# Kernel tuning notes

Hardware: AMD Instinct MI355X
Metric: run time of the kernel (lower is better)

## Reference

```python
import jax, jax.numpy as jnp
import numpy as np

N_BATCH, N_SEQ, N_CHANNELS = 32, 4096, 128
N_EXPERTS, TOP_K = 64, 2
D_IN = 2 * N_SEQ  # linear input width


def setup_inputs() -> dict:
    key = jax.random.key(0)
    k_x, k_wm, k_bm, k_wn, k_bn = jax.random.split(key, 5)
    scale = 1.0 / np.sqrt(D_IN)  # torch nn.Linear default init range
    return {
        "x": jax.random.normal(k_x, (N_BATCH, N_SEQ, N_CHANNELS, 2), dtype=jnp.float32),
        "W_main": jax.random.uniform(k_wm, (N_EXPERTS, D_IN), jnp.float32, -scale, scale),
        "b_main": jax.random.uniform(k_bm, (N_EXPERTS,), jnp.float32, -scale, scale),
        "W_noise": jax.random.uniform(k_wn, (N_EXPERTS, D_IN), jnp.float32, -scale, scale),
        "b_noise": jax.random.uniform(k_bn, (N_EXPERTS,), jnp.float32, -scale, scale),
    }


def _keep_top_k(logits, k):
    # torch.kthvalue(x, n-k) = (n-k)-th smallest (1-based) = sorted[:, n-k-1]
    n = logits.shape[1]
    if n < k:
        return logits
    kth = jnp.sort(logits, axis=1)[:, n - k - 1:n - k]  # [rows, 1]
    return jnp.where(logits > kth, logits, -jnp.inf)


def reference(x, W_main, b_main, W_noise, b_noise):
    n_batch, n_seq, n_channels, _ = x.shape
    # swapaxes(1,2) then reshape -> rows=[batch*channels], feat=[seq*2]
    x_r = jnp.swapaxes(x, 1, 2).reshape(n_batch * n_channels, 2 * n_seq)
    main_out = x_r @ W_main.T + b_main                      # [rows, E]
    noise_out = jax.nn.softplus(x_r @ W_noise.T + b_noise)  # [rows, E]
    gate = _keep_top_k(main_out + noise_out, TOP_K)
    return jax.nn.softmax(gate, axis=1)
```

## Files before the change

kernel.cpp:

```cpp
#include <hip/hip_runtime.h>
#include <cmath>

typedef _Float16 f16x8 __attribute__((ext_vector_type(8)));
typedef _Float16 f16x4 __attribute__((ext_vector_type(4)));
typedef float    f32x16 __attribute__((ext_vector_type(16)));

constexpr int NBATCH = 32;
constexpr int NSEQ   = 4096;
constexpr int NCH    = 128;
constexpr int NEXP   = 64;
constexpr int NE2    = 128;
constexpr int DIN    = 2 * NSEQ;
constexpr int ROWS   = NBATCH * NCH;
constexpr int KCH    = 16;
constexpr float LOSC = 2048.0f;
constexpr float INV_LOSC = 1.0f / 2048.0f;

#define SWZ(row, k) ((((row) * 64) + (k)) ^ (((row) & 7) << 3))

__global__ __launch_bounds__(256, 2)
void gemm_kernel(const float* __restrict__ x,
                 const float* __restrict__ Wm,
                 const float* __restrict__ Wn,
                 float* __restrict__ partials)
{
    const int kc   = blockIdx.x;
    const int b    = blockIdx.y;
    const int tid  = threadIdx.x;
    const int lane = tid & 63;
    const int wave = tid >> 6;
    const int wm   = wave >> 1;
    const int wn   = wave & 1;

    __shared__ _Float16 lds[4 * 8192];
    _Float16* Ah = lds;
    _Float16* Al = lds + 8192;
    _Float16* Bh = lds + 16384;
    _Float16* Bl = lds + 24576;

    f32x16 acc1[2][2], acc2[2][2];
#pragma unroll
    for (int mi = 0; mi < 2; ++mi)
#pragma unroll
        for (int ni = 0; ni < 2; ++ni)
#pragma unroll
            for (int r = 0; r < 16; ++r) { acc1[mi][ni][r] = 0.f; acc2[mi][ni][r] = 0.f; }

    const float* xchunk = x + (size_t)b * (NSEQ * 256) + (size_t)kc * 256 * 256;
    const int fb = kc * 512;

    float2 xr[16];
    auto load_x = [&](int ss) {
        const float* bp = xchunk + ss * 8192;
#pragma unroll
        for (int u = 0; u < 4; ++u) {
            const int kg = u * 2 + (tid >> 7);
#pragma unroll
            for (int j = 0; j < 4; ++j)
                xr[u * 4 + j] = *(const float2*)(bp + (kg * 4 + j) * 256 + (tid & 127) * 2);
        }
    };

    load_x(0);

    for (int ss = 0; ss < 8; ++ss) {
        float4 wr[8];
#pragma unroll
        for (int p = 0; p < 8; ++p) {
            const int e = p * 16 + (tid >> 4);
            const float* wsrc = (e < NEXP) ? (Wm + (size_t)e * DIN)
                                           : (Wn + (size_t)(e - NEXP) * DIN);
            wr[p] = *(const float4*)(wsrc + fb + ss * 64 + (tid & 15) * 4);
        }

        if (ss) __syncthreads();

#pragma unroll
        for (int u = 0; u < 4; ++u) {
            const int kg = u * 2 + (tid >> 7);
            const int c  = tid & 127;
            f16x8 hv, lv;
#pragma unroll
            for (int i = 0; i < 8; ++i) {
                float v = (i & 1) ? xr[u * 4 + (i >> 1)].y : xr[u * 4 + (i >> 1)].x;
                _Float16 h = (_Float16)v;
                hv[i] = h;
                lv[i] = (_Float16)((v - (float)h) * LOSC);
            }
            const int hw = SWZ(c, kg * 8);
            *(f16x8*)&Ah[hw] = hv;
            *(f16x8*)&Al[hw] = lv;
        }
#pragma unroll
        for (int p = 0; p < 8; ++p) {
            const int e = p * 16 + (tid >> 4);
            float vv[4] = { wr[p].x, wr[p].y, wr[p].z, wr[p].w };
            f16x4 hv, lv;
#pragma unroll
            for (int i = 0; i < 4; ++i) {
                _Float16 h = (_Float16)vv[i];
                hv[i] = h;
                lv[i] = (_Float16)((vv[i] - (float)h) * LOSC);
            }
            const int hw = SWZ(e, (tid & 15) * 4);
            *(f16x4*)&Bh[hw] = hv;
            *(f16x4*)&Bl[hw] = lv;
        }
        __syncthreads();

        if (ss < 7) load_x(ss + 1);

#pragma unroll
        for (int kk = 0; kk < 4; ++kk) {
            const int ko = kk * 16 + (lane >> 5) * 8;
            f16x8 ah[2], al[2], bh[2], bl[2];
#pragma unroll
            for (int i = 0; i < 2; ++i) {
                const int ra = wm * 64 + i * 32 + (lane & 31);
                const int rb = wn * 64 + i * 32 + (lane & 31);
                ah[i] = *(const f16x8*)&Ah[SWZ(ra, ko)];
                al[i] = *(const f16x8*)&Al[SWZ(ra, ko)];
                bh[i] = *(const f16x8*)&Bh[SWZ(rb, ko)];
                bl[i] = *(const f16x8*)&Bl[SWZ(rb, ko)];
            }
#pragma unroll
            for (int mi = 0; mi < 2; ++mi)
#pragma unroll
                for (int ni = 0; ni < 2; ++ni) {
                    acc1[mi][ni] = __builtin_amdgcn_mfma_f32_32x32x16_f16(ah[mi], bh[ni], acc1[mi][ni], 0, 0, 0);
                    acc2[mi][ni] = __builtin_amdgcn_mfma_f32_32x32x16_f16(ah[mi], bl[ni], acc2[mi][ni], 0, 0, 0);
                    acc2[mi][ni] = __builtin_amdgcn_mfma_f32_32x32x16_f16(al[mi], bh[ni], acc2[mi][ni], 0, 0, 0);
                }
        }
    }

    float* outp = partials + ((size_t)kc * ROWS + (size_t)b * NCH) * NE2;
#pragma unroll
    for (int mi = 0; mi < 2; ++mi)
#pragma unroll
        for (int ni = 0; ni < 2; ++ni)
#pragma unroll
            for (int r = 0; r < 16; ++r) {
                const int rloc = (r & 3) + 8 * (r >> 2) + 4 * (lane >> 5);
                const int crow = wm * 64 + mi * 32 + rloc;
                const int e    = wn * 64 + ni * 32 + (lane & 31);
                outp[(size_t)crow * NE2 + e] = acc1[mi][ni][r] + acc2[mi][ni][r] * INV_LOSC;
            }
}

__global__ __launch_bounds__(256)
void gate_kernel(const float* __restrict__ partials,
                 const float* __restrict__ bm,
                 const float* __restrict__ bn,
                 float* __restrict__ out)
{
    const int tid  = threadIdx.x;
    const int rl   = tid >> 7;
    const int e    = tid & 127;
    const int lane = tid & 63;
    const int row  = blockIdx.x * 2 + rl;

    const float* p = partials + (size_t)row * NE2 + e;
    float s = 0.f;
#pragma unroll
    for (int kc = 0; kc < KCH; ++kc)
        s += p[(size_t)kc * ROWS * NE2];

    __shared__ float spl[2][64];
    if (e >= NEXP) {
        float nz = s + bn[lane];
        spl[rl][lane] = fmaxf(nz, 0.f) + log1pf(expf(-fabsf(nz)));
    }
    __syncthreads();
    if (e < NEXP) {
        float g = s + bm[lane] + spl[rl][lane];

        float v  = g;
        float m1 = v;
#pragma unroll
        for (int o = 32; o > 0; o >>= 1) m1 = fmaxf(m1, __shfl_xor(m1, o));
        unsigned long long b1 = __ballot(v == m1);
        int l1 = __ffsll(b1) - 1;
        if (lane == l1) v = -INFINITY;
        float m2 = v;
#pragma unroll
        for (int o = 32; o > 0; o >>= 1) m2 = fmaxf(m2, __shfl_xor(m2, o));
        unsigned long long b2 = __ballot(v == m2);
        int l2 = __ffsll(b2) - 1;
        if (lane == l2) v = -INFINITY;
        float kth = v;
#pragma unroll
        for (int o = 32; o > 0; o >>= 1) kth = fmaxf(kth, __shfl_xor(kth, o));

        float ev  = (g > kth) ? expf(g - m1) : 0.f;
        float den = ev;
#pragma unroll
        for (int o = 32; o > 0; o >>= 1) den += __shfl_xor(den, o);
        out[(size_t)row * NEXP + lane] = ev / den;
    }
}

extern "C" void kernel_launch(void* const* d_in, const int* in_sizes, int n_in,
                              void* d_out, int out_size, void* d_ws, size_t ws_size,
                              hipStream_t stream)
{
    const float* x  = (const float*)d_in[0];
    const float* Wm = (const float*)d_in[1];
    const float* bm = (const float*)d_in[2];
    const float* Wn = (const float*)d_in[3];
    const float* bn = (const float*)d_in[4];
    float* out      = (float*)d_out;
    float* partials = (float*)d_ws;

    dim3 g1(KCH, NBATCH);
    gemm_kernel<<<g1, 256, 0, stream>>>(x, Wm, Wn, partials);
    gate_kernel<<<ROWS / 2, 256, 0, stream>>>(partials, bm, bn, out);
}
```

Baseline: 211.9 us.

## Pre-split weights to fp16 hi/lo and double-buffer LDS with direct global-to-LDS loads

Adds a prep kernel that converts both weight matrices once into swizzled fp16 hi/lo arrays in workspace. The GEMM then streams those arrays straight into LDS with global_load_lds and uses two LDS buffers with smaller K tiles, so the next tile's loads overlap the current tile's MFMAs. Block indices are remapped so that neighbouring blocks share batch and chunk data. This removes the per-block weight conversion and the serialised load/compute steps, at the cost of an extra kernel launch and extra workspace traffic.

```diff
diff --git a/kernel.cpp b/kernel.cpp
--- a/kernel.cpp
+++ b/kernel.cpp
@@ -13,30 +13,65 @@
 constexpr int DIN    = 2 * NSEQ;
 constexpr int ROWS   = NBATCH * NCH;
 constexpr int KCH    = 16;
+constexpr int KT     = 16;
 constexpr float LOSC = 2048.0f;
 constexpr float INV_LOSC = 1.0f / 2048.0f;
 
-#define SWZ(row, k) ((((row) * 64) + (k)) ^ (((row) & 7) << 3))
+constexpr size_t WS_WHI = 32ull << 20;
+constexpr size_t WS_WLO = 34ull << 20;
+
+__device__ __forceinline__ int swz_f16(int row, int g) {
+    return row * 32 + ((g ^ ((row >> 1) & 3)) << 3);
+}
+
+__device__ __forceinline__ void gload_lds16(const void* g, void* l) {
+    __builtin_amdgcn_global_load_lds(
+        (const __attribute__((address_space(1))) unsigned int*)g,
+        (__attribute__((address_space(3))) unsigned int*)l, 16, 0, 0);
+}
+
+__global__ __launch_bounds__(256)
+void wprep_kernel(const float* __restrict__ Wm, const float* __restrict__ Wn,
+                  _Float16* __restrict__ Whi, _Float16* __restrict__ Wlo)
+{
+    const int idx = (blockIdx.x * 256 + threadIdx.x) * 4;
+    const int row = idx >> 13;
+    const int f   = idx & 8191;
+    const float* src = (row < NEXP) ? (Wm + (size_t)row * DIN + f)
+                                    : (Wn + (size_t)(row - NEXP) * DIN + f);
+    const float4 v = *(const float4*)src;
+    const int g  = (f >> 3) & 3;
+    const int fs = (f & ~0x18) | ((g ^ ((row >> 1) & 3)) << 3);
+    float vv[4] = { v.x, v.y, v.z, v.w };
+    f16x4 h, l;
+#pragma unroll
+    for (int j = 0; j < 4; ++j) {
+        _Float16 hj = (_Float16)vv[j];
+        h[j] = hj;
+        l[j] = (_Float16)((vv[j] - (float)hj) * LOSC);
+    }
+    *(f16x4*)&Whi[(size_t)row * 8192 + fs] = h;
+    *(f16x4*)&Wlo[(size_t)row * 8192 + fs] = l;
+}
 
 __global__ __launch_bounds__(256, 2)
 void gemm_kernel(const float* __restrict__ x,
-                 const float* __restrict__ Wm,
-                 const float* __restrict__ Wn,
+                 const _Float16* __restrict__ Whi,
+                 const _Float16* __restrict__ Wlo,
                  float* __restrict__ partials)
 {
-    const int kc   = blockIdx.x;
-    const int b    = blockIdx.y;
+    const int l    = blockIdx.x;
+    const int slot = l >> 3;
+    const int kc   = (l & 7) + 8 * (slot & 1);
+    const int b    = slot >> 1;
+
     const int tid  = threadIdx.x;
     const int lane = tid & 63;
     const int wave = tid >> 6;
     const int wm   = wave >> 1;
     const int wn   = wave & 1;
 
-    __shared__ _Float16 lds[4 * 8192];
-    _Float16* Ah = lds;
-    _Float16* Al = lds + 8192;
-    _Float16* Bh = lds + 16384;
-    _Float16* Bl = lds + 24576;
+    __shared__ _Float16 lds[2 * 16384];
 
     f32x16 acc1[2][2], acc2[2][2];
 #pragma unroll
@@ -46,82 +81,81 @@
 #pragma unroll
             for (int r = 0; r < 16; ++r) { acc1[mi][ni][r] = 0.f; acc2[mi][ni][r] = 0.f; }
 
-    const float* xchunk = x + (size_t)b * (NSEQ * 256) + (size_t)kc * 256 * 256;
-    const int fb = kc * 512;
-
-    float2 xr[16];
-    auto load_x = [&](int ss) {
-        const float* bp = xchunk + ss * 8192;
-#pragma unroll
-        for (int u = 0; u < 4; ++u) {
-            const int kg = u * 2 + (tid >> 7);
-#pragma unroll
-            for (int j = 0; j < 4; ++j)
-                xr[u * 4 + j] = *(const float2*)(bp + (kg * 4 + j) * 256 + (tid & 127) * 2);
+    const float* xchunk = x + (size_t)b * (NSEQ * 256) + (size_t)kc * (256 * 256);
+    const int c    = tid & 127;
+    const int gsel = tid >> 7;
+    const int fb0  = kc * 512;
+
+    const int e_ld = lane >> 2;
+    const int goff = (lane & 3) * 8;
+
+    float2 xr[8];
+    auto load_x = [&](int t) {
+#pragma unroll
+        for (int u = 0; u < 2; ++u) {
+            const int g = u * 2 + gsel;
+#pragma unroll
+            for (int i = 0; i < 4; ++i)
+                xr[u * 4 + i] = *(const float2*)(xchunk + (size_t)(t * 16 + g * 4 + i) * 256 + c * 2);
         }
     };
-
+    auto write_x = [&](int buf) {
+        _Float16* Ah = lds + buf * 16384;
+        _Float16* Al = Ah + 4096;
+#pragma unroll
+        for (int u = 0; u < 2; ++u) {
+            const int g = u * 2 + gsel;
+            f16x8 h, lo;
+#pragma unroll
+            for (int i = 0; i < 4; ++i) {
+                float a0 = xr[u * 4 + i].x, a1 = xr[u * 4 + i].y;
+                _Float16 h0 = (_Float16)a0, h1 = (_Float16)a1;
+                h[2 * i] = h0; h[2 * i + 1] = h1;
+                lo[2 * i]     = (_Float16)((a0 - (float)h0) * LOSC);
+                lo[2 * i + 1] = (_Float16)((a1 - (float)h1) * LOSC);
+            }
+            const int off = swz_f16(c, g);
+            *(f16x8*)&Ah[off] = h;
+            *(f16x8*)&Al[off] = lo;
+        }
+    };
+    auto issue_W = [&](int t, int buf) {
+        const int fb = fb0 + t * 32;
+        _Float16* Bh = lds + buf * 16384 + 8192;
+        _Float16* Bl = Bh + 4096;
+#pragma unroll
+        for (int q = 0; q < 2; ++q) {
+            const int e0 = wave * 32 + q * 16;
+            gload_lds16(Whi + (size_t)(e0 + e_ld) * 8192 + fb + goff, Bh + e0 * 32);
+            gload_lds16(Wlo + (size_t)(e0 + e_ld) * 8192 + fb + goff, Bl + e0 * 32);
+        }
+    };
+
+    issue_W(0, 0);
     load_x(0);
-
-    for (int ss = 0; ss < 8; ++ss) {
-        float4 wr[8];
-#pragma unroll
-        for (int p = 0; p < 8; ++p) {
-            const int e = p * 16 + (tid >> 4);
-            const float* wsrc = (e < NEXP) ? (Wm + (size_t)e * DIN)
-                                           : (Wn + (size_t)(e - NEXP) * DIN);
-            wr[p] = *(const float4*)(wsrc + fb + ss * 64 + (tid & 15) * 4);
-        }
-
-        if (ss) __syncthreads();
-
-#pragma unroll
-        for (int u = 0; u < 4; ++u) {
-            const int kg = u * 2 + (tid >> 7);
-            const int c  = tid & 127;
-            f16x8 hv, lv;
-#pragma unroll
-            for (int i = 0; i < 8; ++i) {
-                float v = (i & 1) ? xr[u * 4 + (i >> 1)].y : xr[u * 4 + (i >> 1)].x;
-                _Float16 h = (_Float16)v;
-                hv[i] = h;
-                lv[i] = (_Float16)((v - (float)h) * LOSC);
-            }
-            const int hw = SWZ(c, kg * 8);
-            *(f16x8*)&Ah[hw] = hv;
-            *(f16x8*)&Al[hw] = lv;
-        }
-#pragma unroll
-        for (int p = 0; p < 8; ++p) {
-            const int e = p * 16 + (tid >> 4);
-            float vv[4] = { wr[p].x, wr[p].y, wr[p].z, wr[p].w };
-            f16x4 hv, lv;
-#pragma unroll
-            for (int i = 0; i < 4; ++i) {
-                _Float16 h = (_Float16)vv[i];
-                hv[i] = h;
-                lv[i] = (_Float16)((vv[i] - (float)h) * LOSC);
-            }
-            const int hw = SWZ(e, (tid & 15) * 4);
-            *(f16x4*)&Bh[hw] = hv;
-            *(f16x4*)&Bl[hw] = lv;
-        }
-        __syncthreads();
-
-        if (ss < 7) load_x(ss + 1);
-
-#pragma unroll
-        for (int kk = 0; kk < 4; ++kk) {
-            const int ko = kk * 16 + (lane >> 5) * 8;
+    write_x(0);
+    __syncthreads();
+
+    for (int t = 0; t < KT; ++t) {
+        const int buf = t & 1;
+        if (t < KT - 1) { issue_W(t + 1, buf ^ 1); load_x(t + 1); }
+
+        const _Float16* Ah = lds + buf * 16384;
+        const _Float16* Al = Ah + 4096;
+        const _Float16* Bh = Ah + 8192;
+        const _Float16* Bl = Ah + 12288;
+#pragma unroll
+        for (int kk = 0; kk < 2; ++kk) {
+            const int gk = kk * 2 + (lane >> 5);
             f16x8 ah[2], al[2], bh[2], bl[2];
 #pragma unroll
             for (int i = 0; i < 2; ++i) {
-                const int ra = wm * 64 + i * 32 + (lane & 31);
-                const int rb = wn * 64 + i * 32 + (lane & 31);
-                ah[i] = *(const f16x8*)&Ah[SWZ(ra, ko)];
-                al[i] = *(const f16x8*)&Al[SWZ(ra, ko)];
-                bh[i] = *(const f16x8*)&Bh[SWZ(rb, ko)];
-                bl[i] = *(const f16x8*)&Bl[SWZ(rb, ko)];
+                const int oa = swz_f16(wm * 64 + i * 32 + (lane & 31), gk);
+                const int ob = swz_f16(wn * 64 + i * 32 + (lane & 31), gk);
+                ah[i] = *(const f16x8*)&Ah[oa];
+                al[i] = *(const f16x8*)&Al[oa];
+                bh[i] = *(const f16x8*)&Bh[ob];
+                bl[i] = *(const f16x8*)&Bl[ob];
             }
 #pragma unroll
             for (int mi = 0; mi < 2; ++mi)
@@ -132,6 +166,8 @@
                     acc2[mi][ni] = __builtin_amdgcn_mfma_f32_32x32x16_f16(al[mi], bh[ni], acc2[mi][ni], 0, 0, 0);
                 }
         }
+        if (t < KT - 1) write_x(buf ^ 1);
+        __syncthreads();
     }
 
     float* outp = partials + ((size_t)kc * ROWS + (size_t)b * NCH) * NE2;
@@ -210,9 +246,12 @@
     const float* Wn = (const float*)d_in[3];
     const float* bn = (const float*)d_in[4];
     float* out      = (float*)d_out;
-    float* partials = (float*)d_ws;
-
-    dim3 g1(KCH, NBATCH);
-    gemm_kernel<<<g1, 256, 0, stream>>>(x, Wm, Wn, partials);
+
+    float*     partials = (float*)d_ws;
+    _Float16*  Whi      = (_Float16*)((char*)d_ws + WS_WHI);
+    _Float16*  Wlo      = (_Float16*)((char*)d_ws + WS_WLO);
+
+    wprep_kernel<<<1024, 256, 0, stream>>>(Wm, Wn, Whi, Wlo);
+    gemm_kernel<<<512, 256, 0, stream>>>(x, Whi, Wlo, partials);
     gate_kernel<<<ROWS / 2, 256, 0, stream>>>(partials, bm, bn, out);
 }
```

After: 210.3 us. About the same (-0.8%).
